# Optimization experiments

Measured on AMD Instinct MI355X. Metric: run time of the kernel, lower is better.

Reference implementation:

```python
import jax, jax.numpy as jnp
import numpy as np

D = 512
H = 8
B, S = 4, 2048


def _layernorm(x, g, b, eps=1e-6):
    m = jnp.mean(x, axis=-1, keepdims=True)
    v = jnp.mean(jnp.square(x - m), axis=-1, keepdims=True)
    return (x - m) * jax.lax.rsqrt(v + eps) * g + b


def setup_inputs() -> dict:
    key = jax.random.key(0)
    ks = jax.random.split(key, 8)
    w = 1.0 / np.sqrt(D)  # glorot-ish scale so softmax doesn't saturate
    return {
        "x": jax.random.normal(ks[0], (B, S, D), dtype=jnp.float32),
        "Q": jax.random.normal(ks[1], (H, D, D), dtype=jnp.float32) * w,
        "K": jax.random.normal(ks[2], (H, D, D), dtype=jnp.float32) * w,
        "g1": jnp.ones((D,), jnp.float32),
        "beta1": jnp.zeros((D,), jnp.float32),
        "Wp": jax.random.normal(ks[3], (H * D, D), dtype=jnp.float32) / np.sqrt(H * D),
        "bp": jnp.zeros((D,), jnp.float32),
        "g2": jnp.ones((D,), jnp.float32),
        "beta2": jnp.zeros((D,), jnp.float32),
        "W1": jax.random.normal(ks[4], (D, 4 * D), dtype=jnp.float32) * w,
        "b1": jnp.zeros((4 * D,), jnp.float32),
        "W2": jax.random.normal(ks[5], (4 * D, D), dtype=jnp.float32) / np.sqrt(4 * D),
        "b2": jnp.zeros((D,), jnp.float32),
    }


def reference(x, Q, K, g1, beta1, Wp, bp, g2, beta2, W1, b1, W2, b2):
    # layernorm1
    xn = _layernorm(x, g1, beta1)  # [B,S,D]
    # per-head attention, batched over heads via einsum
    Qx = jnp.einsum("bsd,hde->hbse", xn, Q)  # [H,B,S,D]
    Kx = jnp.einsum("bsd,hde->hbse", xn, K)  # [H,B,S,D]
    scale = 1.0 / jnp.sqrt(jnp.float32(D))
    A = jnp.einsum("hbse,hbte->hbst", Qx, Kx) * scale  # [H,B,S,S]
    A = jax.nn.softmax(A, axis=-1)
    head = jnp.einsum("hbst,btd->hbsd", A, xn) + xn  # per-head residual
    # concat heads along last axis: order h0,h1,... -> [B,S,H*D]
    cat = jnp.transpose(head, (1, 2, 0, 3)).reshape(x.shape[0], x.shape[1], -1)
    # projection
    y = cat @ Wp + bp  # [B,S,D]
    # layernorm2
    y = _layernorm(y, g2, beta2)
    # MLP with residual, exact gelu (keras default)
    h = jax.nn.gelu(y @ W1 + b1, approximate=False)
    h = jax.nn.gelu(h @ W2 + b2, approximate=False)
    return y + h
```

## Files before the change

### kernel.cpp

```cpp
#include <hip/hip_runtime.h>

using u16 = unsigned short;
typedef u16 u16x8 __attribute__((ext_vector_type(8)));
typedef __bf16 bf16x8 __attribute__((ext_vector_type(8)));
typedef float f32x4 __attribute__((ext_vector_type(4)));

__device__ __forceinline__ u16 f2bf(float f) {
  unsigned u = __builtin_bit_cast(unsigned, f);
  u += 0x7fffu + ((u >> 16) & 1u);
  return (u16)(u >> 16);
}
__device__ __forceinline__ float bf2f(u16 h) {
  unsigned u = ((unsigned)h) << 16;
  return __builtin_bit_cast(float, u);
}
__device__ __forceinline__ f32x4 mfma16(u16x8 a, u16x8 b, f32x4 c) {
  return __builtin_amdgcn_mfma_f32_16x16x32_bf16(
      __builtin_bit_cast(bf16x8, a), __builtin_bit_cast(bf16x8, b), c, 0, 0, 0);
}
__device__ __forceinline__ float gelu_f(float v) {
  return 0.5f * v * (1.0f + erff(v * 0.70710678118654752f));
}
__device__ __forceinline__ void gll16(const u16* g, u16* l) {
  __builtin_amdgcn_global_load_lds(
      (const __attribute__((address_space(1))) unsigned*)g,
      (__attribute__((address_space(3))) unsigned*)l, 16, 0, 0);
}

__device__ __forceinline__ float loadf(const float* p) { return *p; }
__device__ __forceinline__ float loadf(const u16* p) { return bf2f(*p); }

template <typename T>
__global__ void tcast_kernel(const T* __restrict__ in, u16* __restrict__ out, int R, int C,
                             float scale) {
  __shared__ float tile[32][33];
  const T* ip = in + (size_t)blockIdx.z * R * C;
  u16* op = out + (size_t)blockIdx.z * R * C;
  int c0 = blockIdx.x * 32, r0 = blockIdx.y * 32;
  int tx = threadIdx.x, ty = threadIdx.y;
#pragma unroll
  for (int i = 0; i < 32; i += 8)
    tile[ty + i][tx] = loadf(ip + (size_t)(r0 + ty + i) * C + (c0 + tx));
  __syncthreads();
#pragma unroll
  for (int i = 0; i < 32; i += 8)
    op[(size_t)(c0 + ty + i) * R + (r0 + tx)] = f2bf(tile[tx][ty + i] * scale);
}

__global__ void vtile_kernel(const u16* __restrict__ in, u16* __restrict__ out) {
  __shared__ u16 tile[32][33];
  const int b = blockIdx.z;
  const int d0 = blockIdx.x * 32, t0 = blockIdx.y * 32;
  const int tx = threadIdx.x, ty = threadIdx.y;
  const u16* ip = in + (size_t)b * 2048 * 512;
#pragma unroll
  for (int i = 0; i < 32; i += 8)
    tile[ty + i][tx] = ip[(size_t)(t0 + ty + i) * 512 + d0 + tx];
  __syncthreads();
  u16* op = out + ((size_t)b * 64 + (t0 >> 5)) * 16384;
#pragma unroll
  for (int i = 0; i < 32; i += 8) {
    const int d = d0 + ty + i;
    op[(size_t)(tx >> 3) * 4096 + (size_t)d * 8 + (tx & 7)] = tile[tx][ty + i];
  }
}

__global__ __launch_bounds__(256) void ln_kernel(
    const float* __restrict__ x, const float* __restrict__ g, const float* __restrict__ b,
    u16* __restrict__ obf, float* __restrict__ of32) {
  const int D = 512;
  int row = blockIdx.x;
  const float* xr = x + (size_t)row * D;
  float2 v = ((const float2*)xr)[threadIdx.x];
  float s = v.x + v.y;
#pragma unroll
  for (int o = 1; o < 64; o <<= 1) s += __shfl_xor(s, o);
  __shared__ float red[4];
  int wid = threadIdx.x >> 6;
  if ((threadIdx.x & 63) == 0) red[wid] = s;
  __syncthreads();
  float mean = (red[0] + red[1] + red[2] + red[3]) * (1.0f / D);
  float dx = v.x - mean, dy = v.y - mean;
  float q = dx * dx + dy * dy;
#pragma unroll
  for (int o = 1; o < 64; o <<= 1) q += __shfl_xor(q, o);
  __syncthreads();
  if ((threadIdx.x & 63) == 0) red[wid] = q;
  __syncthreads();
  float var = (red[0] + red[1] + red[2] + red[3]) * (1.0f / D);
  float rstd = rsqrtf(var + 1e-6f);
  int c = threadIdx.x * 2;
  float o0 = dx * rstd * g[c] + b[c];
  float o1 = dy * rstd * g[c + 1] + b[c + 1];
  obf[(size_t)row * D + c] = f2bf(o0);
  obf[(size_t)row * D + c + 1] = f2bf(o1);
  if (of32 != nullptr) {
    of32[(size_t)row * D + c] = o0;
    of32[(size_t)row * D + c + 1] = o1;
  }
}

__global__ __launch_bounds__(256) void gemm_kernel(
    const u16* __restrict__ A, const u16* __restrict__ Bt,
    const float* __restrict__ bias, const float* __restrict__ resid,
    void* __restrict__ Cout, int M, int N, int K, int mode,
    size_t sA, size_t sB, size_t sC, size_t aHS) {
  __shared__ u16 As[128 * 64];
  __shared__ u16 Bs[128 * 64];
  A += (size_t)blockIdx.z * sA;
  Bt += (size_t)blockIdx.z * sB;
  const size_t zC = (size_t)blockIdx.z * sC;
  const int m0 = blockIdx.y * 128, n0 = blockIdx.x * 128;
  const int tid = threadIdx.x;
  const int l = tid & 63, wv = tid >> 6;
  const int wr = (wv >> 1) * 64, wc = (wv & 1) * 64;
  const int lr = l & 15, lq = l >> 4;
  const int srow = l >> 3;
  const int sc = l & 7;
  f32x4 z4 = {0.f, 0.f, 0.f, 0.f};
  f32x4 acc[4][4];
#pragma unroll
  for (int mi = 0; mi < 4; mi++)
#pragma unroll
    for (int ni = 0; ni < 4; ni++) acc[mi][ni] = z4;

  for (int k0 = 0; k0 < K; k0 += 64) {
    __syncthreads();
#pragma unroll
    for (int j = 0; j < 4; ++j) {
      const int r = wv * 32 + j * 8 + srow;
      const int kc = (sc ^ (r & 7)) * 8;
      const u16* asrc;
      if (aHS) asrc = A + (size_t)(k0 >> 9) * aHS + (size_t)(m0 + r) * 512 + ((k0 & 511) + kc);
      else asrc = A + (size_t)(m0 + r) * K + k0 + kc;
      gll16(asrc, &As[(wv * 32 + j * 8) * 64]);
      const u16* bsrc = Bt + (size_t)(n0 + r) * K + k0 + kc;
      gll16(bsrc, &Bs[(wv * 32 + j * 8) * 64]);
    }
    asm volatile("s_waitcnt vmcnt(0)" ::: "memory");
    __syncthreads();
#pragma unroll
    for (int kk = 0; kk < 2; ++kk) {
      const int rc = ((kk * 4 + lq) ^ (lr & 7)) * 8;
      u16x8 af[4], bfr[4];
#pragma unroll
      for (int mi = 0; mi < 4; mi++) af[mi] = *(const u16x8*)&As[(wr + mi * 16 + lr) * 64 + rc];
#pragma unroll
      for (int ni = 0; ni < 4; ni++) bfr[ni] = *(const u16x8*)&Bs[(wc + ni * 16 + lr) * 64 + rc];
#pragma unroll
      for (int mi = 0; mi < 4; mi++)
#pragma unroll
        for (int ni = 0; ni < 4; ni++) acc[mi][ni] = mfma16(af[mi], bfr[ni], acc[mi][ni]);
    }
  }
#pragma unroll
  for (int mi = 0; mi < 4; mi++) {
#pragma unroll
    for (int ni = 0; ni < 4; ni++) {
      const int gn = n0 + wc + ni * 16 + lr;
      const float bv = (mode != 0 && bias != nullptr) ? bias[gn] : 0.0f;
#pragma unroll
      for (int r = 0; r < 4; r++) {
        const int gm = m0 + wr + mi * 16 + (l >> 4) * 4 + r;
        float v = acc[mi][ni][r];
        const size_t idx = zC + (size_t)gm * N + gn;
        if (mode == 0) ((u16*)Cout)[idx] = f2bf(v);
        else if (mode == 1) ((float*)Cout)[idx] = v + bv;
        else if (mode == 2) ((u16*)Cout)[idx] = f2bf(gelu_f(v + bv));
        else ((float*)Cout)[idx] = gelu_f(v + bv) + resid[(size_t)gm * N + gn];
      }
    }
  }
}

__global__ __launch_bounds__(512, 2) void flash_kernel(
    const u16* __restrict__ Qx, const u16* __restrict__ Kx,
    const u16* __restrict__ xnTt, const u16* __restrict__ xn,
    u16* __restrict__ headout) {
  __shared__ u16 Ks[2][32][512];
  __shared__ u16 Ps[128][40];
  __shared__ float fLds[128];
  __shared__ float lLds[128];

  const int tid = threadIdx.x;
  const int l = tid & 63, wv = tid >> 6;
  const int lr = l & 15, lq = l >> 4, lk8 = lq * 8;
  const int r7 = lr & 7;
  const int h = blockIdx.y >> 2, b = blockIdx.y & 3;
  const int s0 = blockIdx.x * 128;
  const size_t rowHB = (size_t)h * 8192 + (size_t)b * 2048;
  const u16* Qbase = Qx + (rowHB + s0) * 512;
  const u16* Kbase = Kx + rowHB * 512;
  const u16* Vbatch = xnTt + (size_t)b * 64 * 16384;
  const u16* xnb = xn + ((size_t)b * 2048 + s0) * 512;

  u16x8 q[16];
  {
    const u16* qr = Qbase + (size_t)(wv * 16 + lr) * 512 + lk8;
#pragma unroll
    for (int ks = 0; ks < 16; ks++) q[ks] = *(const u16x8*)(qr + ks * 32);
  }
  f32x4 z4 = {0.f, 0.f, 0.f, 0.f};
  f32x4 o[8][4];
#pragma unroll
  for (int mi = 0; mi < 8; mi++)
#pragma unroll
    for (int ni = 0; ni < 4; ni++) o[mi][ni] = z4;
  float m_r[4], l_r[4];
#pragma unroll
  for (int r = 0; r < 4; r++) { m_r[r] = -1e30f; l_r[r] = 0.f; }

#define STAGE(buf, tt0)                                                      \
  do {                                                                       \
    _Pragma("unroll") for (int j = 0; j < 4; ++j) {                          \
      const int row_ = wv * 4 + j;                                           \
      gll16(Kbase + (size_t)((tt0) + row_) * 512 + ((l ^ (row_ & 7)) * 8),   \
            &Ks[buf][row_][0]);                                              \
    }                                                                        \
  } while (0)

  STAGE(0, 0);
  for (int it = 0; it < 64; ++it) {
    const int cur = it & 1;
    asm volatile("s_waitcnt vmcnt(0)" ::: "memory");
    __builtin_amdgcn_s_barrier();
    __builtin_amdgcn_sched_barrier(0);
    STAGE(cur ^ 1, (size_t)((it + 1) & 63) * 32);
    __builtin_amdgcn_sched_barrier(0);
    f32x4 sv0 = z4, sv1 = z4;
    __builtin_amdgcn_s_setprio(1);
#pragma unroll
    for (int ks = 0; ks < 16; ks++) {
      const int col = (((ks << 2) | lq) ^ r7) << 3;
      u16x8 kb0 = *(const u16x8*)&Ks[cur][lr][col];
      u16x8 kb1 = *(const u16x8*)&Ks[cur][16 + lr][col];
      sv0 = mfma16(q[ks], kb0, sv0);
      sv1 = mfma16(q[ks], kb1, sv1);
    }
    __builtin_amdgcn_s_setprio(0);
    float tm[4], fac[4];
#pragma unroll
    for (int r = 0; r < 4; r++) tm[r] = fmaxf(sv0[r], sv1[r]);
#pragma unroll
    for (int r = 0; r < 4; r++) {
      tm[r] = fmaxf(tm[r], __shfl_xor(tm[r], 1));
      tm[r] = fmaxf(tm[r], __shfl_xor(tm[r], 2));
      tm[r] = fmaxf(tm[r], __shfl_xor(tm[r], 4));
      tm[r] = fmaxf(tm[r], __shfl_xor(tm[r], 8));
    }
#pragma unroll
    for (int r = 0; r < 4; r++) {
      float mn = fmaxf(m_r[r], tm[r]);
      fac[r] = __expf(m_r[r] - mn);
      m_r[r] = mn;
      float p0 = __expf(sv0[r] - mn);
      float p1 = __expf(sv1[r] - mn);
      const int prow = wv * 16 + lq * 4 + r;
      Ps[prow][lr] = f2bf(p0);
      Ps[prow][16 + lr] = f2bf(p1);
      float rs = p0 + p1;
      rs += __shfl_xor(rs, 1);
      rs += __shfl_xor(rs, 2);
      rs += __shfl_xor(rs, 4);
      rs += __shfl_xor(rs, 8);
      l_r[r] = l_r[r] * fac[r] + rs;
    }
    if (lr == 0) {
#pragma unroll
      for (int r = 0; r < 4; r++) fLds[wv * 16 + lq * 4 + r] = fac[r];
    }
    asm volatile("s_waitcnt lgkmcnt(0)" ::: "memory");
    __builtin_amdgcn_s_barrier();
    __builtin_amdgcn_sched_barrier(0);
    const u16* Vt_ = Vbatch + (size_t)it * 16384;
    u16x8 vb[4];
#pragma unroll
    for (int ni = 0; ni < 4; ni++)
      vb[ni] = *(const u16x8*)(Vt_ + lq * 4096 + (size_t)(wv * 64 + ni * 16 + lr) * 8);
    __builtin_amdgcn_sched_barrier(0);
#pragma unroll
    for (int mi = 0; mi < 8; mi++) {
#pragma unroll
      for (int r = 0; r < 4; r++) {
        const float fv = fLds[mi * 16 + lq * 4 + r];
#pragma unroll
        for (int ni = 0; ni < 4; ni++) o[mi][ni][r] *= fv;
      }
    }
    asm volatile("s_waitcnt vmcnt(4)" ::: "memory");
    __builtin_amdgcn_sched_barrier(0);
    __builtin_amdgcn_s_setprio(1);
#pragma unroll
    for (int mi = 0; mi < 8; mi++) {
      u16x8 pa = *(const u16x8*)&Ps[mi * 16 + lr][lk8];
#pragma unroll
      for (int ni = 0; ni < 4; ni++) o[mi][ni] = mfma16(pa, vb[ni], o[mi][ni]);
    }
    __builtin_amdgcn_s_setprio(0);
  }
#undef STAGE
  asm volatile("s_waitcnt vmcnt(0)" ::: "memory");
  if (lr == 0) {
#pragma unroll
    for (int r = 0; r < 4; r++) lLds[wv * 16 + lq * 4 + r] = l_r[r];
  }
  __syncthreads();
  u16* outp = headout + (rowHB + s0) * 512;
#pragma unroll
  for (int mi = 0; mi < 8; mi++) {
#pragma unroll
    for (int r = 0; r < 4; r++) {
      const int row = mi * 16 + lq * 4 + r;
      const float linv = 1.0f / lLds[row];
      const u16* xr = xnb + (size_t)row * 512;
      u16* orow = outp + (size_t)row * 512;
#pragma unroll
      for (int ni = 0; ni < 4; ni++) {
        const int c = wv * 64 + ni * 16 + lr;
        orow[c] = f2bf(o[mi][ni][r] * linv + bf2f(xr[c]));
      }
    }
  }
}

extern "C" void kernel_launch(void* const* d_in, const int* in_sizes, int n_in,
                              void* d_out, int out_size, void* d_ws, size_t ws_size,
                              hipStream_t stream) {
  (void)in_sizes; (void)n_in; (void)out_size; (void)ws_size;
  const float* x   = (const float*)d_in[0];
  const float* Qw  = (const float*)d_in[1];
  const float* Kw  = (const float*)d_in[2];
  const float* g1  = (const float*)d_in[3];
  const float* be1 = (const float*)d_in[4];
  const float* Wp  = (const float*)d_in[5];
  const float* bp  = (const float*)d_in[6];
  const float* g2  = (const float*)d_in[7];
  const float* be2 = (const float*)d_in[8];
  const float* W1  = (const float*)d_in[9];
  const float* b1  = (const float*)d_in[10];
  const float* W2  = (const float*)d_in[11];
  const float* b2  = (const float*)d_in[12];
  float* out = (float*)d_out;

  u16* ws = (u16*)d_ws;
  size_t off = 0;
  u16* Qt   = ws + off; off += 8ull * 512 * 512;
  u16* Kt   = ws + off; off += 8ull * 512 * 512;
  u16* Wpt  = ws + off; off += 512ull * 4096;
  u16* W1t  = ws + off; off += 2048ull * 512;
  u16* W2t  = ws + off; off += 512ull * 2048;
  u16* xnb  = ws + off; off += 8192ull * 512;
  u16* xnTt = ws + off; off += 4ull * 512 * 2048;
  u16* Qx   = ws + off; off += 8ull * 8192 * 512;
  u16* Kx   = ws + off; off += 8ull * 8192 * 512;
  u16* yn   = ws + off; off += 8192ull * 512;
  float* y   = (float*)(ws + off); off += 8192ull * 512 * 2;
  float* ynf = (float*)(ws + off); off += 8192ull * 512 * 2;
  u16* h1 = Qx;

  const float qscale = 0.04419417382415922f;
  dim3 tb(32, 8);
  tcast_kernel<float><<<dim3(16, 16, 8), tb, 0, stream>>>(Qw, Qt, 512, 512, qscale);
  tcast_kernel<float><<<dim3(16, 16, 8), tb, 0, stream>>>(Kw, Kt, 512, 512, 1.0f);
  tcast_kernel<float><<<dim3(16, 128, 1), tb, 0, stream>>>(Wp, Wpt, 4096, 512, 1.0f);
  tcast_kernel<float><<<dim3(64, 16, 1), tb, 0, stream>>>(W1, W1t, 512, 2048, 1.0f);
  tcast_kernel<float><<<dim3(16, 64, 1), tb, 0, stream>>>(W2, W2t, 2048, 512, 1.0f);
  ln_kernel<<<8192, 256, 0, stream>>>(x, g1, be1, xnb, nullptr);
  vtile_kernel<<<dim3(16, 64, 4), tb, 0, stream>>>(xnb, xnTt);
  gemm_kernel<<<dim3(4, 64, 16), 256, 0, stream>>>(xnb, Qt, nullptr, nullptr, Qx,
      8192, 512, 512, 0, 0, 262144, 4194304, 0);
  flash_kernel<<<dim3(16, 32), 512, 0, stream>>>(Qx, Kx, xnTt, xnb, Qx);
  gemm_kernel<<<dim3(4, 64, 1), 256, 0, stream>>>(Qx, Wpt, bp, nullptr, y,
      8192, 512, 4096, 1, 0, 0, 0, 4194304);
  ln_kernel<<<8192, 256, 0, stream>>>(y, g2, be2, yn, ynf);
  gemm_kernel<<<dim3(16, 64, 1), 256, 0, stream>>>(yn, W1t, b1, nullptr, h1,
      8192, 2048, 512, 2, 0, 0, 0, 0);
  gemm_kernel<<<dim3(4, 64, 1), 256, 0, stream>>>(h1, W2t, b2, ynf, out,
      8192, 512, 2048, 3, 0, 0, 0, 0);
}
```

Before: 938.7 us.

## Fold Q·Kᵀ into per-head matrix to skip K projection; split-K projection GEMM

Precomputes a per-head fused weight M_h = Q_h K_hᵀ (scaled) with a small batched GEMM. Only xn·M_h is materialised, and the flash kernel uses xn directly as keys, so the per-head K projection and its large Kx buffer disappear. The output projection GEMM is also split along K into two z-slices whose partial sums are added inside the second layernorm kernel, which doubles the grid for that GEMM. The cost is an extra tiny GEMM, a second bf16 rounding of the fused weight, and a larger fp32 staging buffer.

```diff
diff --git a/kernel.cpp b/kernel.cpp
--- a/kernel.cpp
+++ b/kernel.cpp
@@ -25,6 +25,16 @@
   __builtin_amdgcn_global_load_lds(
       (const __attribute__((address_space(1))) unsigned*)g,
       (__attribute__((address_space(3))) unsigned*)l, 16, 0, 0);
+}
+
+__global__ void cast_kernel(const float* __restrict__ in, u16* __restrict__ out,
+                            float scale) {
+  const size_t i = ((size_t)blockIdx.x * 256 + threadIdx.x) * 4;
+  float4 v = *(const float4*)(in + i);
+  out[i] = f2bf(v.x * scale);
+  out[i + 1] = f2bf(v.y * scale);
+  out[i + 2] = f2bf(v.z * scale);
+  out[i + 3] = f2bf(v.w * scale);
 }
 
 __device__ __forceinline__ float loadf(const float* p) { return *p; }
@@ -66,12 +76,18 @@
 }
 
 __global__ __launch_bounds__(256) void ln_kernel(
-    const float* __restrict__ x, const float* __restrict__ g, const float* __restrict__ b,
+    const float* __restrict__ x, const float* __restrict__ x2,
+    const float* __restrict__ g, const float* __restrict__ b,
     u16* __restrict__ obf, float* __restrict__ of32) {
   const int D = 512;
   int row = blockIdx.x;
   const float* xr = x + (size_t)row * D;
   float2 v = ((const float2*)xr)[threadIdx.x];
+  if (x2 != nullptr) {
+    float2 v2 = ((const float2*)(x2 + (size_t)row * D))[threadIdx.x];
+    v.x += v2.x;
+    v.y += v2.y;
+  }
   float s = v.x + v.y;
 #pragma unroll
   for (int o = 1; o < 64; o <<= 1) s += __shfl_xor(s, o);
@@ -103,7 +119,7 @@
 __global__ __launch_bounds__(256) void gemm_kernel(
     const u16* __restrict__ A, const u16* __restrict__ Bt,
     const float* __restrict__ bias, const float* __restrict__ resid,
-    void* __restrict__ Cout, int M, int N, int K, int mode,
+    void* __restrict__ Cout, int M, int N, int K, int ldB, int mode,
     size_t sA, size_t sB, size_t sC, size_t aHS) {
   __shared__ u16 As[128 * 64];
   __shared__ u16 Bs[128 * 64];
@@ -134,7 +150,7 @@
       if (aHS) asrc = A + (size_t)(k0 >> 9) * aHS + (size_t)(m0 + r) * 512 + ((k0 & 511) + kc);
       else asrc = A + (size_t)(m0 + r) * K + k0 + kc;
       gll16(asrc, &As[(wv * 32 + j * 8) * 64]);
-      const u16* bsrc = Bt + (size_t)(n0 + r) * K + k0 + kc;
+      const u16* bsrc = Bt + (size_t)(n0 + r) * ldB + k0 + kc;
       gll16(bsrc, &Bs[(wv * 32 + j * 8) * 64]);
     }
     asm volatile("s_waitcnt vmcnt(0)" ::: "memory");
@@ -158,7 +174,7 @@
 #pragma unroll
     for (int ni = 0; ni < 4; ni++) {
       const int gn = n0 + wc + ni * 16 + lr;
-      const float bv = (mode != 0 && bias != nullptr) ? bias[gn] : 0.0f;
+      const float bv = (mode != 0 && bias != nullptr && blockIdx.z == 0) ? bias[gn] : 0.0f;
 #pragma unroll
       for (int r = 0; r < 4; r++) {
         const int gm = m0 + wr + mi * 16 + (l >> 4) * 4 + r;
@@ -190,7 +206,7 @@
   const int s0 = blockIdx.x * 128;
   const size_t rowHB = (size_t)h * 8192 + (size_t)b * 2048;
   const u16* Qbase = Qx + (rowHB + s0) * 512;
-  const u16* Kbase = Kx + rowHB * 512;
+  const u16* Kbase = Kx + (size_t)b * 2048 * 512;
   const u16* Vbatch = xnTt + (size_t)b * 64 * 16384;
   const u16* xnb = xn + ((size_t)b * 2048 + s0) * 512;
 
@@ -344,37 +360,39 @@
 
   u16* ws = (u16*)d_ws;
   size_t off = 0;
-  u16* Qt   = ws + off; off += 8ull * 512 * 512;
-  u16* Kt   = ws + off; off += 8ull * 512 * 512;
+  u16* Qc   = ws + off; off += 8ull * 512 * 512;
+  u16* Kc   = ws + off; off += 8ull * 512 * 512;
+  u16* Mht  = ws + off; off += 8ull * 512 * 512;
   u16* Wpt  = ws + off; off += 512ull * 4096;
   u16* W1t  = ws + off; off += 2048ull * 512;
   u16* W2t  = ws + off; off += 512ull * 2048;
   u16* xnb  = ws + off; off += 8192ull * 512;
   u16* xnTt = ws + off; off += 4ull * 512 * 2048;
   u16* Qx   = ws + off; off += 8ull * 8192 * 512;
-  u16* Kx   = ws + off; off += 8ull * 8192 * 512;
   u16* yn   = ws + off; off += 8192ull * 512;
-  float* y   = (float*)(ws + off); off += 8192ull * 512 * 2;
+  float* y   = (float*)(ws + off); off += 8192ull * 512 * 4;
   float* ynf = (float*)(ws + off); off += 8192ull * 512 * 2;
   u16* h1 = Qx;
 
   const float qscale = 0.04419417382415922f;
   dim3 tb(32, 8);
-  tcast_kernel<float><<<dim3(16, 16, 8), tb, 0, stream>>>(Qw, Qt, 512, 512, qscale);
-  tcast_kernel<float><<<dim3(16, 16, 8), tb, 0, stream>>>(Kw, Kt, 512, 512, 1.0f);
+  cast_kernel<<<2048, 256, 0, stream>>>(Qw, Qc, qscale);
+  cast_kernel<<<2048, 256, 0, stream>>>(Kw, Kc, 1.0f);
   tcast_kernel<float><<<dim3(16, 128, 1), tb, 0, stream>>>(Wp, Wpt, 4096, 512, 1.0f);
   tcast_kernel<float><<<dim3(64, 16, 1), tb, 0, stream>>>(W1, W1t, 512, 2048, 1.0f);
   tcast_kernel<float><<<dim3(16, 64, 1), tb, 0, stream>>>(W2, W2t, 2048, 512, 1.0f);
-  ln_kernel<<<8192, 256, 0, stream>>>(x, g1, be1, xnb, nullptr);
+  ln_kernel<<<8192, 256, 0, stream>>>(x, nullptr, g1, be1, xnb, nullptr);
   vtile_kernel<<<dim3(16, 64, 4), tb, 0, stream>>>(xnb, xnTt);
-  gemm_kernel<<<dim3(4, 64, 16), 256, 0, stream>>>(xnb, Qt, nullptr, nullptr, Qx,
-      8192, 512, 512, 0, 0, 262144, 4194304, 0);
-  flash_kernel<<<dim3(16, 32), 512, 0, stream>>>(Qx, Kx, xnTt, xnb, Qx);
-  gemm_kernel<<<dim3(4, 64, 1), 256, 0, stream>>>(Qx, Wpt, bp, nullptr, y,
-      8192, 512, 4096, 1, 0, 0, 0, 4194304);
-  ln_kernel<<<8192, 256, 0, stream>>>(y, g2, be2, yn, ynf);
+  gemm_kernel<<<dim3(4, 4, 8), 256, 0, stream>>>(Kc, Qc, nullptr, nullptr, Mht,
+      512, 512, 512, 512, 0, 262144, 262144, 262144, 0);
+  gemm_kernel<<<dim3(4, 64, 8), 256, 0, stream>>>(xnb, Mht, nullptr, nullptr, Qx,
+      8192, 512, 512, 512, 0, 0, 262144, 4194304, 0);
+  flash_kernel<<<dim3(16, 32), 512, 0, stream>>>(Qx, xnb, xnTt, xnb, Qx);
+  gemm_kernel<<<dim3(4, 64, 2), 256, 0, stream>>>(Qx, Wpt, bp, nullptr, y,
+      8192, 512, 2048, 4096, 1, 16777216, 2048, 4194304, 4194304);
+  ln_kernel<<<8192, 256, 0, stream>>>(y, y + 4194304, g2, be2, yn, ynf);
   gemm_kernel<<<dim3(16, 64, 1), 256, 0, stream>>>(yn, W1t, b1, nullptr, h1,
-      8192, 2048, 512, 2, 0, 0, 0, 0);
+      8192, 2048, 512, 512, 2, 0, 0, 0, 0);
   gemm_kernel<<<dim3(4, 64, 1), 256, 0, stream>>>(h1, W2t, b2, ynf, out,
-      8192, 512, 2048, 3, 0, 0, 0, 0);
-}
+      8192, 512, 2048, 2048, 3, 0, 0, 0, 0);
+}
```

Result: faster. 865.6 us (-7.8%).
